# Kernel optimization log

Measured on AMD Instinct MI355X. Metric: run time of the kernel, lower is better.

The kernel has to match this reference:

```python
import jax, jax.numpy as jnp
import numpy as np

EMBED = 256
HEADS = 8
LEVELS = 4
POINTS = 4
HD = EMBED // HEADS  # 32
SHAPES = np.array([[100, 100], [50, 50], [25, 25], [13, 13]], dtype=np.int64)  # (H_l, W_l)


def setup_inputs() -> dict:
    key = jax.random.key(0)
    ks = jax.random.split(key, 12)
    nv = int(SHAPES.prod(-1).sum())  # 13294
    bs, nq, d = 2, nv, EMBED
    level_start = np.concatenate([[0], SHAPES.prod(-1).cumsum()[:-1]])
    s = 0.02
    return {
        "query": jax.random.normal(ks[0], (bs, nq, d), jnp.float32),
        "reference_points": jax.random.uniform(ks[1], (bs, nq, LEVELS, 2), jnp.float32),
        "value": jax.random.normal(ks[2], (bs, nv, d), jnp.float32),
        "spatial_shapes": jnp.asarray(SHAPES, jnp.int32),
        "level_start_index": jnp.asarray(level_start, jnp.int32),
        "key_padding_mask": jnp.zeros((bs, nv), jnp.bool_),
        "W_samp": jax.random.normal(ks[3], (HEADS * LEVELS * POINTS * 2, d), jnp.float32) * s,
        "b_samp": jax.random.normal(ks[4], (HEADS * LEVELS * POINTS * 2,), jnp.float32),
        "W_attn": jax.random.normal(ks[5], (HEADS * LEVELS * POINTS, d), jnp.float32) * s,
        "b_attn": jnp.zeros((HEADS * LEVELS * POINTS,), jnp.float32),
        "W_val": jax.random.normal(ks[6], (d, d), jnp.float32) * s,
        "b_val": jnp.zeros((d,), jnp.float32),
        "W_out": jax.random.normal(ks[7], (d, d), jnp.float32) * s,
        "b_out": jnp.zeros((d,), jnp.float32),
    }


def _msda_core(value_bhnd, shapes_np, starts_np, loc, attn):
    """value_bhnd: (bs, H, nv, hd); loc: (bs, nq, H, L, P, 2) in [0,1]; attn: (bs, nq, H, L, P)."""
    bs, heads, nv, hd = value_bhnd.shape
    nq = loc.shape[1]
    out = jnp.zeros((bs, nq, heads, hd), value_bhnd.dtype)
    for l in range(LEVELS):
        H, W = int(shapes_np[l, 0]), int(shapes_np[l, 1])
        start = int(starts_np[l])
        v = jax.lax.dynamic_slice_in_dim(value_bhnd, start, H * W, axis=2)  # (bs, heads, H*W, hd)
        # grid_sample(align_corners=False): pixel coord = loc * size - 0.5
        lx = loc[:, :, :, l, :, 0] * W - 0.5  # (bs, nq, heads, P)
        ly = loc[:, :, :, l, :, 1] * H - 0.5
        x0 = jnp.floor(lx)
        y0 = jnp.floor(ly)
        tx = lx - x0
        ty = ly - y0
        x0i = x0.astype(jnp.int32)
        y0i = y0.astype(jnp.int32)
        samp = jnp.zeros((bs, heads, nq, POINTS, hd), value_bhnd.dtype)
        for dy, wy in ((0, 1.0 - ty), (1, ty)):
            for dx, wx in ((0, 1.0 - tx), (1, tx)):
                xi = x0i + dx
                yi = y0i + dy
                valid = (xi >= 0) & (xi < W) & (yi >= 0) & (yi < H)  # zeros padding
                idx = jnp.clip(yi, 0, H - 1) * W + jnp.clip(xi, 0, W - 1)  # (bs, nq, heads, P)
                idx_t = idx.transpose(0, 2, 1, 3).reshape(bs, heads, nq * POINTS)
                g = jnp.take_along_axis(v, idx_t[..., None], axis=2)
                g = g.reshape(bs, heads, nq, POINTS, hd)
                w = jnp.where(valid, wx * wy, 0.0).transpose(0, 2, 1, 3)[..., None]
                samp = samp + g * w
        out = out + jnp.einsum("bhqpd,bqhp->bqhd", samp, attn[:, :, :, l, :])
    return out.reshape(bs, nq, heads * hd)


def reference(query, reference_points, value, spatial_shapes, level_start_index,
              key_padding_mask, W_samp, b_samp, W_attn, b_attn, W_val, b_val, W_out, b_out):
    bs, nq, d = query.shape
    v = value @ W_val.T + b_val
    v = jnp.where(key_padding_mask[..., None], 0.0, v)
    v = v.reshape(bs, -1, HEADS, HD).transpose(0, 2, 1, 3)  # (bs, heads, nv, hd)
    off = (query @ W_samp.T + b_samp).reshape(bs, nq, HEADS, LEVELS, POINTS, 2)
    attn = (query @ W_attn.T + b_attn).reshape(bs, nq, HEADS, LEVELS * POINTS)
    attn = jax.nn.softmax(attn, axis=-1).reshape(bs, nq, HEADS, LEVELS, POINTS)
    ss = np.asarray(spatial_shapes)
    starts = np.asarray(level_start_index)
    # offset normalizer is (W, H) per level
    norm = jnp.asarray(ss[:, ::-1].copy(), jnp.float32)
    loc = reference_points[:, :, None, :, None, :] + off / norm[None, None, None, :, None, :]
    out = _msda_core(v, ss, starts, loc, attn)
    return out @ W_out.T + b_out
```

## Files before the change

### kernel.cpp

```cpp
#include <hip/hip_runtime.h>
#include <hip/hip_bf16.h>
#include <hip/hip_fp16.h>
#include <cstdint>
#include <cstddef>

#define EMBED  256
#define NV_PER_B 13294
#define M_PAD   26624
#define NQPB   8

__constant__ const int c_H[4]  = {100, 50, 25, 13};
__constant__ const int c_W[4]  = {100, 50, 25, 13};
__constant__ const int c_ST[4] = {0, 10000, 12500, 13125};

typedef __attribute__((ext_vector_type(8))) short bf16x8;
typedef __attribute__((ext_vector_type(4))) float f32x4;

__device__ inline short f2bf(float x) {
    __hip_bfloat16 h = __float2bfloat16(x);
    return *reinterpret_cast<short*>(&h);
}

__global__ __launch_bounds__(256) void convert_kernel(
    const float* __restrict__ q,  const float* __restrict__ v,
    const float* __restrict__ wv, const float* __restrict__ wsamp,
    const float* __restrict__ wattn, const float* __restrict__ wo,
    const float* __restrict__ bsamp, const float* __restrict__ battn,
    short* __restrict__ q_bf, short* __restrict__ v_bf,
    short* __restrict__ wv_bf, short* __restrict__ wcat_bf,
    short* __restrict__ wo_bf, float* __restrict__ bias_cat,
    int n_real4, int n_pad4)
{
    const int i = blockIdx.x * 256 + threadIdx.x;
    if (i < n_pad4) {
        float4 a = make_float4(0.f, 0.f, 0.f, 0.f);
        float4 b = make_float4(0.f, 0.f, 0.f, 0.f);
        if (i < n_real4) {
            a = ((const float4*)q)[i];
            b = ((const float4*)v)[i];
        }
        ((short4*)q_bf)[i] = make_short4(f2bf(a.x), f2bf(a.y), f2bf(a.z), f2bf(a.w));
        ((short4*)v_bf)[i] = make_short4(f2bf(b.x), f2bf(b.y), f2bf(b.z), f2bf(b.w));
    }
    if (i < 16384) {
        float4 a = ((const float4*)wv)[i];
        float4 c = ((const float4*)wo)[i];
        ((short4*)wv_bf)[i] = make_short4(f2bf(a.x), f2bf(a.y), f2bf(a.z), f2bf(a.w));
        ((short4*)wo_bf)[i] = make_short4(f2bf(c.x), f2bf(c.y), f2bf(c.z), f2bf(c.w));
    }
    if (i < 24576) {
        float4 a = (i < 16384) ? ((const float4*)wsamp)[i]
                               : ((const float4*)wattn)[i - 16384];
        ((short4*)wcat_bf)[i] = make_short4(f2bf(a.x), f2bf(a.y), f2bf(a.z), f2bf(a.w));
    }
    if (i < 96) {
        float4 a = (i < 64) ? ((const float4*)bsamp)[i]
                            : ((const float4*)battn)[i - 64];
        ((float4*)bias_cat)[i] = a;
    }
}

__device__ __forceinline__ void gemm_kloop(
    const short* __restrict__ A, const short* __restrict__ Wt,
    int bm, int bn, char* smem, f32x4 (&acc)[4][4],
    int t, int wave, int lane)
{
    constexpr int K = 256;
    const int row0 = t >> 2, row1 = row0 + 64;
    const int kbl  = t & 3;
    const int kbg0 = kbl ^ (row0 & 3);
    const int kbg1 = kbl ^ (row1 & 3);
    const size_t a0 = (size_t)(bm + row0) * K + kbg0 * 8;
    const size_t a1 = (size_t)(bm + row1) * K + kbg1 * 8;
    const size_t b0 = (size_t)(bn + row0) * K + kbg0 * 8;
    const size_t b1 = (size_t)(bn + row1) * K + kbg1 * 8;
    const int lr16 = lane & 15, qk = lane >> 4;
    const int swz  = (qk ^ (lr16 & 3)) * 16;
    const int wrow = wave & 1, wcol = wave >> 1;

    auto issue = [&](int stage, int k0) {
        char* sa = smem + stage * 16384 + wave * 1024;
        char* sb = sa + 8192;
        __builtin_amdgcn_global_load_lds(
            (const __attribute__((address_space(1))) void*)(A + a0 + k0),
            (__attribute__((address_space(3))) void*)(sa), 16, 0, 0);
        __builtin_amdgcn_global_load_lds(
            (const __attribute__((address_space(1))) void*)(A + a1 + k0),
            (__attribute__((address_space(3))) void*)(sa + 4096), 16, 0, 0);
        __builtin_amdgcn_global_load_lds(
            (const __attribute__((address_space(1))) void*)(Wt + b0 + k0),
            (__attribute__((address_space(3))) void*)(sb), 16, 0, 0);
        __builtin_amdgcn_global_load_lds(
            (const __attribute__((address_space(1))) void*)(Wt + b1 + k0),
            (__attribute__((address_space(3))) void*)(sb + 4096), 16, 0, 0);
    };

    issue(0, 0);
    #pragma unroll
    for (int it = 0; it < 8; ++it) {
        __syncthreads();
        if (it + 1 < 8) issue((it + 1) & 1, (it + 1) * 32);
        const char* sa = smem + (it & 1) * 16384;
        const char* sb = sa + 8192;
        bf16x8 af[4], bfr[4];
        #pragma unroll
        for (int mi = 0; mi < 4; ++mi)
            af[mi] = *(const bf16x8*)(sa + (wrow * 64 + mi * 16 + lr16) * 64 + swz);
        #pragma unroll
        for (int ni = 0; ni < 4; ++ni)
            bfr[ni] = *(const bf16x8*)(sb + (wcol * 64 + ni * 16 + lr16) * 64 + swz);
        #pragma unroll
        for (int mi = 0; mi < 4; ++mi)
            #pragma unroll
            for (int ni = 0; ni < 4; ++ni)
                acc[mi][ni] = __builtin_amdgcn_mfma_f32_16x16x32_bf16(
                    af[mi], bfr[ni], acc[mi][ni], 0, 0, 0);
    }
}

__global__ __launch_bounds__(256) void gemm_mega_kernel(
    const short* __restrict__ v_bf, const short* __restrict__ wv_bf,
    const float* __restrict__ b_val, __half* __restrict__ vproj,
    const short* __restrict__ q_bf, const short* __restrict__ wcat_bf,
    const float* __restrict__ bias_cat, __half* __restrict__ qo)
{
    __shared__ __align__(16) char smem[36864];
    const int t = threadIdx.x;
    const int wave = t >> 6, lane = t & 63;
    const int lr16 = lane & 15, qk = lane >> 4;
    const int wrow = wave & 1, wcol = wave >> 1;
    const int y = blockIdx.y;
    const int bm = blockIdx.x * 128;

    const short* A; const short* Wt; const float* bias; __half* Cc; int Nst, bn;
    if (y < 2) { A = v_bf; Wt = wv_bf;   bias = b_val;    Cc = vproj; Nst = 256; bn = y * 128; }
    else       { A = q_bf; Wt = wcat_bf; bias = bias_cat; Cc = qo;    Nst = 384; bn = (y - 2) * 128; }

    f32x4 acc[4][4] = {};
    gemm_kloop(A, Wt, bm, bn, smem, acc, t, wave, lane);

    __syncthreads();
    __half* ep = (__half*)(smem + wave * 9216);
    const int colbase = bn + wcol * 64;
    float bv[4];
    #pragma unroll
    for (int ni = 0; ni < 4; ++ni) bv[ni] = bias[colbase + ni * 16 + lr16];
    #pragma unroll
    for (int mi = 0; mi < 4; ++mi)
        #pragma unroll
        for (int ni = 0; ni < 4; ++ni)
            #pragma unroll
            for (int r = 0; r < 4; ++r)
                ep[(mi * 16 + qk * 4 + r) * 72 + ni * 16 + lr16] =
                    __float2half(acc[mi][ni][r] + bv[ni]);
    __syncthreads();
    const int er = lane >> 3, ec = (lane & 7) * 8;
    #pragma unroll
    for (int pass = 0; pass < 8; ++pass) {
        const int r = pass * 8 + er;
        const int4 vv = *(const int4*)&ep[r * 72 + ec];
        const int grow = bm + wrow * 64 + r;
        *(int4*)&Cc[(size_t)grow * Nst + colbase + ec] = vv;
    }
}

__global__ __launch_bounds__(256) void gemm_out_kernel(
    const short* __restrict__ corebf, const short* __restrict__ wo_bf,
    const float* __restrict__ b_out, float* __restrict__ C, int M)
{
    __shared__ __align__(16) char smem[36864];
    const int t = threadIdx.x;
    const int wave = t >> 6, lane = t & 63;
    const int lr16 = lane & 15, qk = lane >> 4;
    const int wrow = wave & 1, wcol = wave >> 1;
    const int bm = blockIdx.x * 128, bn = blockIdx.y * 128;

    f32x4 acc[4][4] = {};
    gemm_kloop(corebf, wo_bf, bm, bn, smem, acc, t, wave, lane);

    const int colbase = bn + wcol * 64;
    float bv[4];
    #pragma unroll
    for (int ni = 0; ni < 4; ++ni) bv[ni] = b_out[colbase + ni * 16 + lr16];
    float* ep = (float*)(smem + wave * 8704);
    #pragma unroll
    for (int p = 0; p < 2; ++p) {
        __syncthreads();
        #pragma unroll
        for (int mh = 0; mh < 2; ++mh) {
            const int mi = p * 2 + mh;
            #pragma unroll
            for (int ni = 0; ni < 4; ++ni)
                #pragma unroll
                for (int r = 0; r < 4; ++r)
                    ep[(mh * 16 + qk * 4 + r) * 68 + ni * 16 + lr16] =
                        acc[mi][ni][r] + bv[ni];
        }
        __syncthreads();
        const int er = lane >> 4, ec = (lane & 15) * 4;
        #pragma unroll
        for (int j = 0; j < 8; ++j) {
            const int r = j * 4 + er;
            const float4 vv = *(const float4*)&ep[r * 68 + ec];
            const int grow = bm + wrow * 64 + p * 32 + r;
            if (grow < M)
                *(float4*)&C[(size_t)grow * 256 + colbase + ec] = vv;
        }
    }
}

__global__ __launch_bounds__(256) void msda_core_kernel(
    const __half* __restrict__ vproj,
    const float* __restrict__ refp,
    const __half* __restrict__ qo,
    short* __restrict__ core,
    int nq, int nv, int M)
{
    const int bq0 = blockIdx.x * NQPB;
    const int t = threadIdx.x;

    __shared__ float s_w[NQPB * 128];
    __shared__ float s_ref[NQPB * 8];
    __shared__ unsigned int s_tap[NQPB * 8][65];

    #pragma unroll
    for (int i = 0; i < 4; ++i) {
        const int s = t + i * 256;
        const int q = s >> 7, r = s & 127;
        s_w[s] = __half2float(qo[(size_t)(bq0 + q) * 384 + 256 + r]);
    }
    if (t < NQPB * 8) {
        const int gq = min(bq0 + (t >> 3), M - 1);
        s_ref[t] = refp[(size_t)gq * 8 + (t & 7)];
    }
    __syncthreads();

    if (t < NQPB * 8) {
        const int base = (t >> 3) * 128 + (t & 7) * 16;
        float m = -1e30f;
        #pragma unroll
        for (int j = 0; j < 16; ++j) m = fmaxf(m, s_w[base + j]);
        float e[16]; float ssum = 0.f;
        #pragma unroll
        for (int j = 0; j < 16; ++j) { e[j] = expf(s_w[base + j] - m); ssum += e[j]; }
        const float inv = 1.f / ssum;
        #pragma unroll
        for (int j = 0; j < 16; ++j) s_w[base + j] = e[j] * inv;
    }
    __syncthreads();

    #pragma unroll
    for (int i = 0; i < 4; ++i) {
        const int s = t + i * 256;
        const int q = s >> 7, r = s & 127;
        const int h = r >> 4, lp = r & 15, l = lp >> 2;
        const int gq = bq0 + q;
        const float2 off = __half22float2(*(const __half2*)&qo[(size_t)gq * 384 + r * 2]);
        const float rx = s_ref[q * 8 + l * 2];
        const float ry = s_ref[q * 8 + l * 2 + 1];
        const int W = c_W[l], H = c_H[l], st = c_ST[l];
        const float fW = (float)W, fH = (float)H;
        const float lx = (rx + off.x / fW) * fW - 0.5f;
        const float ly = (ry + off.y / fH) * fH - 0.5f;
        const float x0f = floorf(lx), y0f = floorf(ly);
        const float fx = lx - x0f, fy = ly - y0f;
        const int x0 = (int)x0f, y0 = (int)y0f;
        const float aw = s_w[s];
        const float wx[2] = {1.f - fx, fx};
        const float wy[2] = {1.f - fy, fy};
        #pragma unroll
        for (int dy = 0; dy < 2; ++dy) {
            #pragma unroll
            for (int dx = 0; dx < 2; ++dx) {
                const int xi = x0 + dx, yi = y0 + dy;
                const bool ok = (xi >= 0) & (xi < W) & (yi >= 0) & (yi < H);
                const unsigned int idx = ok ? (unsigned int)(st + yi * W + xi) : 0u;
                const float w = ok ? aw * wy[dy] * wx[dx] : 0.f;
                const unsigned int pw = (unsigned int)__half_as_ushort(__float2half(w));
                s_tap[q * 8 + h][lp * 4 + dy * 2 + dx] = idx | (pw << 16);
            }
        }
    }
    __syncthreads();

    const int q   = t >> 5;
    const int l32 = t & 31;
    const int h   = l32 >> 2;
    const int c8  = l32 & 3;
    const int gq  = bq0 + q;
    const int b   = (gq >= nq) ? 1 : 0;
    const __half* __restrict__ vb = vproj + (size_t)b * nv * EMBED + h * 32 + c8 * 8;
    const unsigned int* __restrict__ taps = s_tap[q * 8 + h];

    float a[8] = {0.f, 0.f, 0.f, 0.f, 0.f, 0.f, 0.f, 0.f};
    #pragma unroll 8
    for (int j = 0; j < 64; ++j) {
        const unsigned int u = taps[j];
        const float w = __half2float(__ushort_as_half((unsigned short)(u >> 16)));
        const int4 raw = *(const int4*)(vb + (size_t)(u & 0xFFFFu) * EMBED);
        const __half2* hh = (const __half2*)&raw;
        float2 f;
        f = __half22float2(hh[0]); a[0] = fmaf(w, f.x, a[0]); a[1] = fmaf(w, f.y, a[1]);
        f = __half22float2(hh[1]); a[2] = fmaf(w, f.x, a[2]); a[3] = fmaf(w, f.y, a[3]);
        f = __half22float2(hh[2]); a[4] = fmaf(w, f.x, a[4]); a[5] = fmaf(w, f.y, a[5]);
        f = __half22float2(hh[3]); a[6] = fmaf(w, f.x, a[6]); a[7] = fmaf(w, f.y, a[7]);
    }

    if (gq < M) {
        __align__(16) short o[8];
        #pragma unroll
        for (int i = 0; i < 8; ++i) o[i] = f2bf(a[i]);
        *(int4*)&core[(size_t)gq * 256 + h * 32 + c8 * 8] = *(const int4*)o;
    }
}

extern "C" void kernel_launch(void* const* d_in, const int* in_sizes, int n_in,
                              void* d_out, int out_size, void* d_ws, size_t ws_size,
                              hipStream_t stream) {
    const float* query  = (const float*)d_in[0];
    const float* refp   = (const float*)d_in[1];
    const float* value  = (const float*)d_in[2];
    const float* W_samp = (const float*)d_in[6];
    const float* b_samp = (const float*)d_in[7];
    const float* W_attn = (const float*)d_in[8];
    const float* b_attn = (const float*)d_in[9];
    const float* W_val  = (const float*)d_in[10];
    const float* b_val  = (const float*)d_in[11];
    const float* W_out  = (const float*)d_in[12];
    const float* b_out  = (const float*)d_in[13];
    float* out = (float*)d_out;

    const int M  = in_sizes[0] / EMBED;
    const int nq = NV_PER_B;
    const int nv = NV_PER_B;
    const int Mp = M_PAD;

    char* p = (char*)d_ws;
    short*  q_bf   = (short*)p;  p += (size_t)Mp * 256 * 2;
    short*  v_bf   = (short*)p;  p += (size_t)Mp * 256 * 2;
    short*  corebf = (short*)p;  p += (size_t)Mp * 256 * 2;
    __half* vproj  = (__half*)p; p += (size_t)Mp * 256 * 2;
    __half* qo     = (__half*)p; p += (size_t)Mp * 384 * 2;
    short*  wv_bf  = (short*)p;  p += 65536 * 2;
    short*  wcat   = (short*)p;  p += 98304 * 2;
    short*  wo_bf  = (short*)p;  p += 65536 * 2;
    float*  biascat= (float*)p;  p += 384 * 4;

    const int n_real4 = M * 256 / 4;
    const int n_pad4  = Mp * 256 / 4;
    dim3 blk(256);

    convert_kernel<<<dim3((n_pad4 + 255) / 256), blk, 0, stream>>>(
        query, value, W_val, W_samp, W_attn, W_out, b_samp, b_attn,
        q_bf, v_bf, wv_bf, wcat, wo_bf, biascat, n_real4, n_pad4);

    const int mb = Mp / 128;
    gemm_mega_kernel<<<dim3(mb, 5), blk, 0, stream>>>(
        v_bf, wv_bf, b_val, vproj, q_bf, wcat, biascat, qo);

    msda_core_kernel<<<dim3((M + NQPB - 1) / NQPB), blk, 0, stream>>>(
        vproj, refp, qo, corebf, nq, nv, M);

    gemm_out_kernel<<<dim3(mb, 2), blk, 0, stream>>>(
        corebf, wo_bf, b_out, out, M);
}
```

Before: 206.6 us.

## Fuse fp32-to-bf16 input conversion into projection GEMM and batch MSDA gathers

Removes the full-size conversion pass that wrote bf16 copies of query and value. The projection GEMM now loads fp32 A tiles into registers, converts them, and writes them to swizzled LDS while the weight tiles still stream through global_load_lds. The MSDA gather loop now reads four packed taps at once from LDS and issues four independent vector loads per group to expose more memory-level parallelism. The cost is register-staged A loads in the GEMM, with extra VGPR pressure and less asynchronous overlap, plus row clamping for the padded rows.

```diff
diff --git a/kernel.cpp b/kernel.cpp
--- a/kernel.cpp
+++ b/kernel.cpp
@@ -6,6 +6,7 @@
 
 #define EMBED  256
 #define NV_PER_B 13294
+#define M_REAL  26588
 #define M_PAD   26624
 #define NQPB   8
 
@@ -21,27 +22,14 @@
     return *reinterpret_cast<short*>(&h);
 }
 
-__global__ __launch_bounds__(256) void convert_kernel(
-    const float* __restrict__ q,  const float* __restrict__ v,
+__global__ __launch_bounds__(256) void wconv_kernel(
     const float* __restrict__ wv, const float* __restrict__ wsamp,
     const float* __restrict__ wattn, const float* __restrict__ wo,
     const float* __restrict__ bsamp, const float* __restrict__ battn,
-    short* __restrict__ q_bf, short* __restrict__ v_bf,
     short* __restrict__ wv_bf, short* __restrict__ wcat_bf,
-    short* __restrict__ wo_bf, float* __restrict__ bias_cat,
-    int n_real4, int n_pad4)
+    short* __restrict__ wo_bf, float* __restrict__ bias_cat)
 {
     const int i = blockIdx.x * 256 + threadIdx.x;
-    if (i < n_pad4) {
-        float4 a = make_float4(0.f, 0.f, 0.f, 0.f);
-        float4 b = make_float4(0.f, 0.f, 0.f, 0.f);
-        if (i < n_real4) {
-            a = ((const float4*)q)[i];
-            b = ((const float4*)v)[i];
-        }
-        ((short4*)q_bf)[i] = make_short4(f2bf(a.x), f2bf(a.y), f2bf(a.z), f2bf(a.w));
-        ((short4*)v_bf)[i] = make_short4(f2bf(b.x), f2bf(b.y), f2bf(b.z), f2bf(b.w));
-    }
     if (i < 16384) {
         float4 a = ((const float4*)wv)[i];
         float4 c = ((const float4*)wo)[i];
@@ -60,7 +48,125 @@
     }
 }
 
-__device__ __forceinline__ void gemm_kloop(
+__global__ __launch_bounds__(256) void proj_gemm_kernel(
+    const float* __restrict__ value, const short* __restrict__ wv_bf,
+    const float* __restrict__ b_val, __half* __restrict__ vproj,
+    const float* __restrict__ query, const short* __restrict__ wcat_bf,
+    const float* __restrict__ bias_cat, __half* __restrict__ qo, int M)
+{
+    constexpr int K = 256;
+    __shared__ __align__(16) char smem[36864];
+
+    const int t = threadIdx.x;
+    const int wave = t >> 6, lane = t & 63;
+    const int lr16 = lane & 15, qk = lane >> 4;
+    const int wrow = wave & 1, wcol = wave >> 1;
+    const int y = blockIdx.y;
+    const int bm = blockIdx.x * 128;
+
+    const float* A; const short* Wt; const float* bias; __half* Cc; int Nst, bn;
+    if (y < 2) { A = value; Wt = wv_bf;   bias = b_val;    Cc = vproj; Nst = 256; bn = y * 128; }
+    else       { A = query; Wt = wcat_bf; bias = bias_cat; Cc = qo;    Nst = 384; bn = (y - 2) * 128; }
+
+    const int arow = t >> 1;
+    const int akh  = (t & 1) * 16;
+    const size_t abase = (size_t)min(bm + arow, M - 1) * K + akh;
+    const int aslot0 = ((t & 1) * 2 + 0) ^ (arow & 3);
+    const int aslot1 = ((t & 1) * 2 + 1) ^ (arow & 3);
+
+    const int brow0 = t >> 2, brow1 = brow0 + 64;
+    const int kbl  = t & 3;
+    const int kbg0 = kbl ^ (brow0 & 3);
+    const int kbg1 = kbl ^ (brow1 & 3);
+    const size_t b0 = (size_t)(bn + brow0) * K + kbg0 * 8;
+    const size_t b1 = (size_t)(bn + brow1) * K + kbg1 * 8;
+    const int swz  = (qk ^ (lr16 & 3)) * 16;
+
+    f32x4 acc[4][4] = {};
+    float4 areg[4];
+
+    auto loadA = [&](int k0) {
+        #pragma unroll
+        for (int i = 0; i < 4; ++i)
+            areg[i] = *(const float4*)&A[abase + k0 + i * 4];
+    };
+    auto issueB = [&](int stage, int k0) {
+        char* sb = smem + stage * 16384 + 8192 + wave * 1024;
+        __builtin_amdgcn_global_load_lds(
+            (const __attribute__((address_space(1))) void*)(Wt + b0 + k0),
+            (__attribute__((address_space(3))) void*)(sb), 16, 0, 0);
+        __builtin_amdgcn_global_load_lds(
+            (const __attribute__((address_space(1))) void*)(Wt + b1 + k0),
+            (__attribute__((address_space(3))) void*)(sb + 4096), 16, 0, 0);
+    };
+    auto writeA = [&](int stage) {
+        char* sa = smem + stage * 16384;
+        __align__(16) short h8a[8], h8b[8];
+        const float* f = (const float*)areg;
+        #pragma unroll
+        for (int i = 0; i < 8; ++i) { h8a[i] = f2bf(f[i]); h8b[i] = f2bf(f[8 + i]); }
+        *(bf16x8*)(sa + arow * 64 + aslot0 * 16) = *(const bf16x8*)h8a;
+        *(bf16x8*)(sa + arow * 64 + aslot1 * 16) = *(const bf16x8*)h8b;
+    };
+
+    loadA(0);
+    issueB(0, 0);
+    writeA(0);
+    #pragma unroll
+    for (int it = 0; it < 8; ++it) {
+        __syncthreads();
+        if (it + 1 < 8) {
+            loadA((it + 1) * 32);
+            issueB((it + 1) & 1, (it + 1) * 32);
+        }
+        const char* sa = smem + (it & 1) * 16384;
+        const char* sb = sa + 8192;
+        bf16x8 af[4], bfr[4];
+        #pragma unroll
+        for (int mi = 0; mi < 4; ++mi) {
+            const int m = wrow * 64 + mi * 16 + lr16;
+            af[mi] = *(const bf16x8*)(sa + m * 64 + ((qk ^ (m & 3)) * 16));
+        }
+        #pragma unroll
+        for (int ni = 0; ni < 4; ++ni) {
+            const int n = wcol * 64 + ni * 16 + lr16;
+            bfr[ni] = *(const bf16x8*)(sb + n * 64 + ((qk ^ (n & 3)) * 16));
+        }
+        #pragma unroll
+        for (int mi = 0; mi < 4; ++mi)
+            #pragma unroll
+            for (int ni = 0; ni < 4; ++ni)
+                acc[mi][ni] = __builtin_amdgcn_mfma_f32_16x16x32_bf16(
+                    af[mi], bfr[ni], acc[mi][ni], 0, 0, 0);
+        if (it + 1 < 8) writeA((it + 1) & 1);
+    }
+
+    __syncthreads();
+    __half* ep = (__half*)(smem + wave * 9216);
+    const int colbase = bn + wcol * 64;
+    float bv[4];
+    #pragma unroll
+    for (int ni = 0; ni < 4; ++ni) bv[ni] = bias[colbase + ni * 16 + lr16];
+    #pragma unroll
+    for (int mi = 0; mi < 4; ++mi)
+        #pragma unroll
+        for (int ni = 0; ni < 4; ++ni)
+            #pragma unroll
+            for (int r = 0; r < 4; ++r)
+                ep[(mi * 16 + qk * 4 + r) * 72 + ni * 16 + lr16] =
+                    __float2half(acc[mi][ni][r] + bv[ni]);
+    __syncthreads();
+    const int er = lane >> 3, ec = (lane & 7) * 8;
+    #pragma unroll
+    for (int pass = 0; pass < 8; ++pass) {
+        const int r = pass * 8 + er;
+        const int4 vv = *(const int4*)&ep[r * 72 + ec];
+        const int grow = bm + wrow * 64 + r;
+        *(int4*)&Cc[(size_t)grow * Nst + colbase + ec] = vv;
+    }
+}
+
+__device__ __forceinline__ void gemm_kloop_bf16(
     const short* __restrict__ A, const short* __restrict__ Wt,
     int bm, int bn, char* smem, f32x4 (&acc)[4][4],
     int t, int wave, int lane)
@@ -75,7 +181,6 @@
     const size_t b0 = (size_t)(bn + row0) * K + kbg0 * 8;
     const size_t b1 = (size_t)(bn + row1) * K + kbg1 * 8;
     const int lr16 = lane & 15, qk = lane >> 4;
-    const int swz  = (qk ^ (lr16 & 3)) * 16;
     const int wrow = wave & 1, wcol = wave >> 1;
 
     auto issue = [&](int stage, int k0) {
@@ -104,63 +209,21 @@
         const char* sb = sa + 8192;
         bf16x8 af[4], bfr[4];
         #pragma unroll
-        for (int mi = 0; mi < 4; ++mi)
-            af[mi] = *(const bf16x8*)(sa + (wrow * 64 + mi * 16 + lr16) * 64 + swz);
-        #pragma unroll
-        for (int ni = 0; ni < 4; ++ni)
-            bfr[ni] = *(const bf16x8*)(sb + (wcol * 64 + ni * 16 + lr16) * 64 + swz);
+        for (int mi = 0; mi < 4; ++mi) {
+            const int m = wrow * 64 + mi * 16 + lr16;
+            af[mi] = *(const bf16x8*)(sa + m * 64 + ((qk ^ (m & 3)) * 16));
+        }
+        #pragma unroll
+        for (int ni = 0; ni < 4; ++ni) {
+            const int n = wcol * 64 + ni * 16 + lr16;
+            bfr[ni] = *(const bf16x8*)(sb + n * 64 + ((qk ^ (n & 3)) * 16));
+        }
         #pragma unroll
         for (int mi = 0; mi < 4; ++mi)
             #pragma unroll
             for (int ni = 0; ni < 4; ++ni)
                 acc[mi][ni] = __builtin_amdgcn_mfma_f32_16x16x32_bf16(
                     af[mi], bfr[ni], acc[mi][ni], 0, 0, 0);
-    }
-}
-
-__global__ __launch_bounds__(256) void gemm_mega_kernel(
-    const short* __restrict__ v_bf, const short* __restrict__ wv_bf,
-    const float* __restrict__ b_val, __half* __restrict__ vproj,
-    const short* __restrict__ q_bf, const short* __restrict__ wcat_bf,
-    const float* __restrict__ bias_cat, __half* __restrict__ qo)
-{
-    __shared__ __align__(16) char smem[36864];
-    const int t = threadIdx.x;
-    const int wave = t >> 6, lane = t & 63;
-    const int lr16 = lane & 15, qk = lane >> 4;
-    const int wrow = wave & 1, wcol = wave >> 1;
-    const int y = blockIdx.y;
-    const int bm = blockIdx.x * 128;
-
-    const short* A; const short* Wt; const float* bias; __half* Cc; int Nst, bn;
-    if (y < 2) { A = v_bf; Wt = wv_bf;   bias = b_val;    Cc = vproj; Nst = 256; bn = y * 128; }
-    else       { A = q_bf; Wt = wcat_bf; bias = bias_cat; Cc = qo;    Nst = 384; bn = (y - 2) * 128; }
-
-    f32x4 acc[4][4] = {};
-    gemm_kloop(A, Wt, bm, bn, smem, acc, t, wave, lane);
-
-    __syncthreads();
-    __half* ep = (__half*)(smem + wave * 9216);
-    const int colbase = bn + wcol * 64;
-    float bv[4];
-    #pragma unroll
-    for (int ni = 0; ni < 4; ++ni) bv[ni] = bias[colbase + ni * 16 + lr16];
-    #pragma unroll
-    for (int mi = 0; mi < 4; ++mi)
-        #pragma unroll
-        for (int ni = 0; ni < 4; ++ni)
-            #pragma unroll
-            for (int r = 0; r < 4; ++r)
-                ep[(mi * 16 + qk * 4 + r) * 72 + ni * 16 + lr16] =
-                    __float2half(acc[mi][ni][r] + bv[ni]);
-    __syncthreads();
-    const int er = lane >> 3, ec = (lane & 7) * 8;
-    #pragma unroll
-    for (int pass = 0; pass < 8; ++pass) {
-        const int r = pass * 8 + er;
-        const int4 vv = *(const int4*)&ep[r * 72 + ec];
-        const int grow = bm + wrow * 64 + r;
-        *(int4*)&Cc[(size_t)grow * Nst + colbase + ec] = vv;
     }
 }
 
@@ -176,7 +239,7 @@
     const int bm = blockIdx.x * 128, bn = blockIdx.y * 128;
 
     f32x4 acc[4][4] = {};
-    gemm_kloop(corebf, wo_bf, bm, bn, smem, acc, t, wave, lane);
+    gemm_kloop_bf16(corebf, wo_bf, bm, bn, smem, acc, t, wave, lane);
 
     const int colbase = bn + wcol * 64;
     float bv[4];
@@ -221,7 +284,7 @@
 
     __shared__ float s_w[NQPB * 128];
     __shared__ float s_ref[NQPB * 8];
-    __shared__ unsigned int s_tap[NQPB * 8][65];
+    __shared__ __align__(16) unsigned int s_tap[NQPB * 8][68];
 
     #pragma unroll
     for (int i = 0; i < 4; ++i) {
@@ -290,20 +353,33 @@
     const int gq  = bq0 + q;
     const int b   = (gq >= nq) ? 1 : 0;
     const __half* __restrict__ vb = vproj + (size_t)b * nv * EMBED + h * 32 + c8 * 8;
-    const unsigned int* __restrict__ taps = s_tap[q * 8 + h];
+    const uint4* __restrict__ tapq = (const uint4*)s_tap[q * 8 + h];
 
     float a[8] = {0.f, 0.f, 0.f, 0.f, 0.f, 0.f, 0.f, 0.f};
-    #pragma unroll 8
-    for (int j = 0; j < 64; ++j) {
-        const unsigned int u = taps[j];
-        const float w = __half2float(__ushort_as_half((unsigned short)(u >> 16)));
-        const int4 raw = *(const int4*)(vb + (size_t)(u & 0xFFFFu) * EMBED);
-        const __half2* hh = (const __half2*)&raw;
-        float2 f;
-        f = __half22float2(hh[0]); a[0] = fmaf(w, f.x, a[0]); a[1] = fmaf(w, f.y, a[1]);
-        f = __half22float2(hh[1]); a[2] = fmaf(w, f.x, a[2]); a[3] = fmaf(w, f.y, a[3]);
-        f = __half22float2(hh[2]); a[4] = fmaf(w, f.x, a[4]); a[5] = fmaf(w, f.y, a[5]);
-        f = __half22float2(hh[3]); a[6] = fmaf(w, f.x, a[6]); a[7] = fmaf(w, f.y, a[7]);
+    uint4 tq = tapq[0];
+    #pragma unroll
+    for (int g = 0; g < 16; ++g) {
+        const int4 r0 = *(const int4*)(vb + (size_t)(tq.x & 0xFFFFu) * EMBED);
+        const int4 r1 = *(const int4*)(vb + (size_t)(tq.y & 0xFFFFu) * EMBED);
+        const int4 r2 = *(const int4*)(vb + (size_t)(tq.z & 0xFFFFu) * EMBED);
+        const int4 r3 = *(const int4*)(vb + (size_t)(tq.w & 0xFFFFu) * EMBED);
+        const uint4 tn = (g < 15) ? tapq[g + 1] : tq;
+        const float w0 = __half2float(__ushort_as_half((unsigned short)(tq.x >> 16)));
+        const float w1 = __half2float(__ushort_as_half((unsigned short)(tq.y >> 16)));
+        const float w2 = __half2float(__ushort_as_half((unsigned short)(tq.z >> 16)));
+        const float w3 = __half2float(__ushort_as_half((unsigned short)(tq.w >> 16)));
+        const __half* g0 = (const __half*)&r0;
+        const __half* g1 = (const __half*)&r1;
+        const __half* g2 = (const __half*)&r2;
+        const __half* g3 = (const __half*)&r3;
+        #pragma unroll
+        for (int i = 0; i < 8; ++i) {
+            a[i] = fmaf(w0, __half2float(g0[i]), a[i]);
+            a[i] = fmaf(w1, __half2float(g1[i]), a[i]);
+            a[i] = fmaf(w2, __half2float(g2[i]), a[i]);
+            a[i] = fmaf(w3, __half2float(g3[i]), a[i]);
+        }
+        tq = tn;
     }
 
     if (gq < M) {
@@ -336,8 +412,6 @@
     const int Mp = M_PAD;
 
     char* p = (char*)d_ws;
-    short*  q_bf   = (short*)p;  p += (size_t)Mp * 256 * 2;
-    short*  v_bf   = (short*)p;  p += (size_t)Mp * 256 * 2;
     short*  corebf = (short*)p;  p += (size_t)Mp * 256 * 2;
     __half* vproj  = (__half*)p; p += (size_t)Mp * 256 * 2;
     __half* qo     = (__half*)p; p += (size_t)Mp * 384 * 2;
@@ -346,17 +420,15 @@
     short*  wo_bf  = (short*)p;  p += 65536 * 2;
     float*  biascat= (float*)p;  p += 384 * 4;
 
-    const int n_real4 = M * 256 / 4;
-    const int n_pad4  = Mp * 256 / 4;
     dim3 blk(256);
 
-    convert_kernel<<<dim3((n_pad4 + 255) / 256), blk, 0, stream>>>(
-        query, value, W_val, W_samp, W_attn, W_out, b_samp, b_attn,
-        q_bf, v_bf, wv_bf, wcat, wo_bf, biascat, n_real4, n_pad4);
+    wconv_kernel<<<dim3(96), blk, 0, stream>>>(
+        W_val, W_samp, W_attn, W_out, b_samp, b_attn,
+        wv_bf, wcat, wo_bf, biascat);
 
     const int mb = Mp / 128;
-    gemm_mega_kernel<<<dim3(mb, 5), blk, 0, stream>>>(
-        v_bf, wv_bf, b_val, vproj, q_bf, wcat, biascat, qo);
+    proj_gemm_kernel<<<dim3(mb, 5), blk, 0, stream>>>(
+        value, wv_bf, b_val, vproj, query, wcat, biascat, qo, M);
 
     msda_core_kernel<<<dim3((M + NQPB - 1) / NQPB), blk, 0, stream>>>(
         vproj, refp, qo, corebf, nq, nv, M);
```

Result: slower. 402.0 us (+94.6%).
